# Optimization experiments

Hardware: AMD Instinct MI355X
Metric: run time of the kernel (lower is better)

The kernel has to match this reference:

```python
import jax, jax.numpy as jnp
import numpy as np

WAVE_LEN = 1000.0
DIM_G = 64


def box_relational_embedding(boxes):
    # boxes: (B, N, 4) -> (B, N, N, 64) trigonometric geometry embedding
    B, N, _ = boxes.shape
    x_min, y_min, x_max, y_max = jnp.split(boxes, 4, axis=-1)  # each (B,N,1)
    cx = (x_min + x_max) * 0.5
    cy = (y_min + y_max) * 0.5
    w = (x_max - x_min) + 1.0
    h = (y_max - y_min) + 1.0
    cxT = jnp.swapaxes(cx, 1, 2)  # (B,1,N)
    cyT = jnp.swapaxes(cy, 1, 2)
    dx = jnp.log(jnp.clip(jnp.abs((cx - cxT) / w), 1e-3))  # (B,N,N)
    dy = jnp.log(jnp.clip(jnp.abs((cy - cyT) / h), 1e-3))
    dw = jnp.log(w / jnp.swapaxes(w, 1, 2))
    dh = jnp.log(h / jnp.swapaxes(h, 1, 2))
    pos = jnp.stack([dx, dy, dw, dh], axis=-1)  # (B,N,N,4)
    n_freq = DIM_G // 8  # 8 frequency bands
    dim_mat = 1.0 / (WAVE_LEN ** (jnp.arange(n_freq, dtype=pos.dtype) / n_freq))
    mul = (100.0 * pos)[..., None] * dim_mat  # (B,N,N,4,8)
    mul = mul.reshape(B, N, N, 4 * n_freq)  # (B,N,N,32)
    return jnp.concatenate([jnp.sin(mul), jnp.cos(mul)], axis=-1)  # (B,N,N,64)


def setup_inputs() -> dict:
    key = jax.random.key(0)
    ks = jax.random.split(key, 12)
    B, N, D, H = 32, 196, 1024, 8
    scale = 0.02
    inp = {
        "input_query": jax.random.normal(ks[0], (B, N, D), jnp.float32),
        "input_key": jax.random.normal(ks[1], (B, N, D), jnp.float32),
        "input_value": jax.random.normal(ks[2], (B, N, D), jnp.float32),
        "input_box": jax.random.uniform(ks[3], (B, N, 4), jnp.float32),
        "Wq": jax.random.normal(ks[4], (D, D), jnp.float32) * scale,
        "bq": jnp.zeros((D,), jnp.float32),
        "Wk": jax.random.normal(ks[5], (D, D), jnp.float32) * scale,
        "bk": jnp.zeros((D,), jnp.float32),
        "Wv": jax.random.normal(ks[6], (D, D), jnp.float32) * scale,
        "bv": jnp.zeros((D,), jnp.float32),
        "Wo": jax.random.normal(ks[7], (D, D), jnp.float32) * scale,
        "bo": jnp.zeros((D,), jnp.float32),
        "WG_w": jax.random.normal(ks[8], (H, DIM_G), jnp.float32) * scale,  # 8 stacked (64->1) linears
        "WG_b": jnp.zeros((H,), jnp.float32),
    }
    return inp


def reference(input_query, input_key, input_value, input_box,
              Wq, bq, Wk, bk, Wv, bv, Wo, bo, WG_w, WG_b):
    B, N, D = input_query.shape
    H = WG_w.shape[0]
    dk = D // H
    # relation geometry weights per head: (B,H,N,N)
    geo = box_relational_embedding(input_box)  # (B,N,N,64)
    wg = jax.nn.relu(jnp.einsum('bnmg,hg->bhnm', geo, WG_w) + WG_b[None, :, None, None])
    # projections (torch Linear: x @ W.T + b), reshape to (B,H,N,dk)
    def proj(x, W, b):
        return (x @ W.T + b).reshape(B, N, H, dk).transpose(0, 2, 1, 3)
    q = proj(input_query, Wq, bq)
    k = proj(input_key, Wk, bk)
    v = proj(input_value, Wv, bv)
    scores = jnp.einsum('bhnd,bhmd->bhnm', q, k) / np.sqrt(dk).astype(q.dtype)
    logits = jnp.log(jnp.clip(wg, 1e-6)) + scores
    attn = jax.nn.softmax(logits, axis=-1)  # (B,H,N,N)
    out = jnp.einsum('bhnm,bhmd->bhnd', attn, v)  # (B,H,N,dk)
    out = out.transpose(0, 2, 1, 3).reshape(B, N, D)
    return out @ Wo.T + bo
```

## Files before the change

kernel.cpp:

```cpp
#include <hip/hip_runtime.h>
#include <hip/hip_bf16.h>

typedef __bf16 bf16;
typedef _Float16 half_t;
typedef bf16 bf16x8 __attribute__((ext_vector_type(8)));
typedef bf16 bf16x4 __attribute__((ext_vector_type(4)));
typedef float floatx4 __attribute__((ext_vector_type(4)));

#define B_ 32
#define N_ 196
#define H_ 8
#define D_ 1024
#define DK_ 128
#define BN_ (B_ * N_)
#define BH_ (B_ * H_)
#define NPAD_ 224
#define PSTRIDE_ 232

#define KT_ 16

typedef __attribute__((address_space(3))) unsigned int lds_uint;
typedef const __attribute__((address_space(1))) unsigned int glb_uint;

__device__ __forceinline__ void async_copy16(const bf16* g, bf16* l) {
  __builtin_amdgcn_global_load_lds((glb_uint*)g, (lds_uint*)l, 16, 0, 0);
}

__device__ __forceinline__ bf16x8 bzero8() {
  bf16x8 z;
#pragma unroll
  for (int i = 0; i < 8; i++) z[i] = (bf16)0.0f;
  return z;
}

#define BARRIER() asm volatile("s_barrier" ::: "memory")
#define WAITV0() asm volatile("s_waitcnt vmcnt(0)" ::: "memory")

__global__ __launch_bounds__(256) void cvt3_kernel(const float* __restrict__ s0,
                                                   const float* __restrict__ s1,
                                                   const float* __restrict__ s2,
                                                   bf16* __restrict__ d0,
                                                   bf16* __restrict__ d1,
                                                   bf16* __restrict__ d2, int n4) {
  const int which = blockIdx.y;
  const float* s = (which == 0) ? s0 : (which == 1) ? s1 : s2;
  bf16* d = (which == 0) ? d0 : (which == 1) ? d1 : d2;
  int i = blockIdx.x * 256 + threadIdx.x;
  if (i >= n4) return;
  float4 v = ((const float4*)s)[i];
  bf16x4 o;
  o[0] = (bf16)v.x;
  o[1] = (bf16)v.y;
  o[2] = (bf16)v.z;
  o[3] = (bf16)v.w;
  *(bf16x4*)(d + (size_t)i * 4) = o;
}

__global__ __launch_bounds__(256) void cvt4_kernel(const float* __restrict__ s0,
                                                   const float* __restrict__ s1,
                                                   const float* __restrict__ s2,
                                                   const float* __restrict__ s3,
                                                   bf16* __restrict__ d0,
                                                   bf16* __restrict__ d1,
                                                   bf16* __restrict__ d2,
                                                   bf16* __restrict__ d3, int n4) {
  const int which = blockIdx.y;
  const float* s = (which == 0) ? s0 : (which == 1) ? s1 : (which == 2) ? s2 : s3;
  bf16* d = (which == 0) ? d0 : (which == 1) ? d1 : (which == 2) ? d2 : d3;
  int i = blockIdx.x * 256 + threadIdx.x;
  if (i >= n4) return;
  float4 v = ((const float4*)s)[i];
  bf16x4 o;
  o[0] = (bf16)v.x;
  o[1] = (bf16)v.y;
  o[2] = (bf16)v.z;
  o[3] = (bf16)v.w;
  *(bf16x4*)(d + (size_t)i * 4) = o;
}

__global__ __launch_bounds__(256) void geo_kernel(const float* __restrict__ box,
                                                  const float* __restrict__ WGw,
                                                  const float* __restrict__ WGb,
                                                  half_t* __restrict__ S) {
  __shared__ float4 wsh[128];
  if (threadIdx.x < 128) wsh[threadIdx.x] = ((const float4*)WGw)[threadIdx.x];
  __syncthreads();

  int tid = blockIdx.x * 256 + threadIdx.x;
  int b = tid / (N_ * N_);
  int rem = tid - b * (N_ * N_);
  int n = rem / N_;
  int m = rem - n * N_;

  float4 bn = ((const float4*)box)[b * N_ + n];
  float4 bm = ((const float4*)box)[b * N_ + m];
  float cxn = (bn.x + bn.z) * 0.5f, cyn = (bn.y + bn.w) * 0.5f;
  float wn = bn.z - bn.x + 1.0f, hn = bn.w - bn.y + 1.0f;
  float cxm = (bm.x + bm.z) * 0.5f, cym = (bm.y + bm.w) * 0.5f;
  float wm = bm.z - bm.x + 1.0f, hm = bm.w - bm.y + 1.0f;

  float pos[4];
  pos[0] = __logf(fmaxf(fabsf((cxn - cxm) / wn), 1e-3f));
  pos[1] = __logf(fmaxf(fabsf((cyn - cym) / hn), 1e-3f));
  pos[2] = __logf(wn / wm);
  pos[3] = __logf(hn / hm);

  const float dims[8] = {1.0f,          0.4216965034f, 0.1778279410f, 0.0749894209f,
                         0.0316227766f, 0.0133352143f, 0.0056234133f, 0.0023713737f};
  float feat[64];
#pragma unroll
  for (int p = 0; p < 4; p++) {
#pragma unroll
    for (int f = 0; f < 8; f++) {
      float a = 100.0f * pos[p] * dims[f];
      feat[p * 8 + f] = __sinf(a);
      feat[32 + p * 8 + f] = __cosf(a);
    }
  }
#pragma unroll
  for (int hh = 0; hh < 8; hh++) {
    float accv = WGb[hh];
#pragma unroll
    for (int g4 = 0; g4 < 16; g4++) {
      float4 wv = wsh[hh * 16 + g4];
      accv += feat[g4 * 4 + 0] * wv.x + feat[g4 * 4 + 1] * wv.y +
              feat[g4 * 4 + 2] * wv.z + feat[g4 * 4 + 3] * wv.w;
    }
    S[((size_t)((b * H_ + hh) * N_ + n)) * NPAD_ + m] = (half_t)fmaxf(accv, 1e-6f);
  }
}

template <int VARIANT>
__global__ __launch_bounds__(256, 2) void gemm2p(
    const bf16* __restrict__ A0, const bf16* __restrict__ A1, const bf16* __restrict__ A2,
    const bf16* __restrict__ W0, const bf16* __restrict__ W1, const bf16* __restrict__ W2,
    const float* __restrict__ b0, const float* __restrict__ b1, const float* __restrict__ b2,
    void* __restrict__ O0, void* __restrict__ O1, void* __restrict__ O2) {
  __shared__ bf16 As[2][128 * 64];
  __shared__ bf16 Bs[2][128 * 64];

  const int z = (VARIANT == 0) ? blockIdx.z : 0;
  const bf16* A = (z == 0) ? A0 : (z == 1) ? A1 : A2;
  const bf16* W = (z == 0) ? W0 : (z == 1) ? W1 : W2;
  const float* bias = (z == 0) ? b0 : (z == 1) ? b1 : b2;

  const int tid = threadIdx.x;
  const int lane = tid & 63;
  const int wid = tid >> 6;
  const int l16 = lane & 15;
  const int quad = lane >> 4;
  const int wm = wid >> 1;
  const int wn = wid & 1;

  const bf16* gA = A + (size_t)blockIdx.y * 128 * D_;
  const bf16* gB = W + (size_t)blockIdx.x * 128 * D_;

  const int srow = tid >> 3;
  const int lslot = (tid & 7) ^ (srow & 7);
  size_t sOff[4];
#pragma unroll
  for (int u = 0; u < 4; u++) sOff[u] = (size_t)(u * 32 + srow) * D_ + lslot * 8;

  int arow[4], brow[4], kslot[2];
#pragma unroll
  for (int i = 0; i < 4; i++) arow[i] = (wm * 64 + i * 16 + l16) * 64;
#pragma unroll
  for (int j = 0; j < 4; j++) brow[j] = (wn * 64 + j * 16 + l16) * 64;
#pragma unroll
  for (int kk = 0; kk < 2; kk++) kslot[kk] = ((kk * 4 + quad) ^ (l16 & 7)) * 8;

  floatx4 acc[4][4];
#pragma unroll
  for (int i = 0; i < 4; i++)
#pragma unroll
    for (int j = 0; j < 4; j++)
#pragma unroll
      for (int r = 0; r < 4; r++) acc[i][j][r] = 0.0f;

#pragma unroll
  for (int u = 0; u < 4; u++) {
    async_copy16(gA + sOff[u], &As[0][u * 2048 + tid * 8]);
    async_copy16(gB + sOff[u], &Bs[0][u * 2048 + tid * 8]);
  }
  WAITV0();
  BARRIER();

  for (int kt = 0; kt < KT_; ++kt) {
    const int cur = kt & 1;
    const bf16* Ab = As[cur];
    const bf16* Bb = Bs[cur];
    const bool pf = (kt + 1 < KT_);
    const bf16* pa = gA + (kt + 1) * 64;
    const bf16* pb = gB + (kt + 1) * 64;
    bf16* dA = As[cur ^ 1];
    bf16* dB = Bs[cur ^ 1];
    bf16x8 af[4], bfv[4];

#pragma unroll
    for (int i = 0; i < 4; i++) af[i] = *(const bf16x8*)(Ab + arow[i] + kslot[0]);
#pragma unroll
    for (int j = 0; j < 4; j++) bfv[j] = *(const bf16x8*)(Bb + brow[j] + kslot[0]);
    if (pf) {
#pragma unroll
      for (int u = 0; u < 4; u++) async_copy16(pa + sOff[u], dA + u * 2048 + tid * 8);
    }
    __builtin_amdgcn_s_setprio(1);
#pragma unroll
    for (int i = 0; i < 4; i++)
#pragma unroll
      for (int j = 0; j < 4; j++)
        acc[i][j] = __builtin_amdgcn_mfma_f32_16x16x32_bf16(af[i], bfv[j], acc[i][j], 0, 0, 0);
    __builtin_amdgcn_s_setprio(0);

#pragma unroll
    for (int i = 0; i < 4; i++) af[i] = *(const bf16x8*)(Ab + arow[i] + kslot[1]);
#pragma unroll
    for (int j = 0; j < 4; j++) bfv[j] = *(const bf16x8*)(Bb + brow[j] + kslot[1]);
    if (pf) {
#pragma unroll
      for (int u = 0; u < 4; u++) async_copy16(pb + sOff[u], dB + u * 2048 + tid * 8);
    }
    __builtin_amdgcn_s_setprio(1);
#pragma unroll
    for (int i = 0; i < 4; i++)
#pragma unroll
      for (int j = 0; j < 4; j++)
        acc[i][j] = __builtin_amdgcn_mfma_f32_16x16x32_bf16(af[i], bfv[j], acc[i][j], 0, 0, 0);
    __builtin_amdgcn_s_setprio(0);

    if (pf) {
      WAITV0();
      BARRIER();
    }
  }

  const int m0 = blockIdx.y * 128 + wm * 64;
  const int n0 = blockIdx.x * 128 + wn * 64;
#pragma unroll
  for (int j = 0; j < 4; j++) {
    const int col = n0 + j * 16 + l16;
    const float bv = bias[col];
#pragma unroll
    for (int i = 0; i < 4; i++) {
#pragma unroll
      for (int r = 0; r < 4; r++) {
        const int row = m0 + i * 16 + quad * 4 + r;
        float v = acc[i][j][r] + bv;
        if (VARIANT == 1) {
          ((float*)O0)[(size_t)row * D_ + col] = v;
        } else if (z < 2) {
          bf16* Cout = z ? (bf16*)O1 : (bf16*)O0;
          Cout[(size_t)row * D_ + col] = (bf16)v;
        } else {
          int b = row / N_;
          int n = row - b * N_;
          int h = col >> 7;
          int d = col & (DK_ - 1);
          ((bf16*)O2)[((size_t)((b * H_ + h) * DK_ + d)) * NPAD_ + n] = (bf16)v;
        }
      }
    }
  }
}

__global__ __launch_bounds__(256) void attn_kernel(const bf16* __restrict__ Q,
                                                   const bf16* __restrict__ Kmat,
                                                   const bf16* __restrict__ Vt,
                                                   const half_t* __restrict__ Sb,
                                                   bf16* __restrict__ AO) {
  __shared__ bf16 Pl[4 * 16 * PSTRIDE_];

  const int f = blockIdx.x;
  const int tile = (f >> 3) & 3;
  const int bh = (f & 7) | ((f >> 5) << 3);
  const int b = bh >> 3;
  const int h = bh & 7;
  const int wave = threadIdx.x >> 6;
  const int lane = threadIdx.x & 63;
  const int l16 = lane & 15;
  const int quad = lane >> 4;
  const int nrb = tile * 64 + wave * 16;

  floatx4 S[14];
#pragma unroll
  for (int j = 0; j < 14; j++)
#pragma unroll
    for (int r = 0; r < 4; r++) S[j][r] = 0.0f;

  const int na = nrb + l16;
  const bool nav = na < N_;
  const bf16* aptr = Q + ((size_t)(b * N_ + (nav ? na : 0))) * D_ + h * DK_ + quad * 8;
  bf16x8 afr[4];
#pragma unroll
  for (int kk = 0; kk < 4; kk++) afr[kk] = nav ? *(const bf16x8*)(aptr + kk * 32) : bzero8();

#pragma unroll
  for (int j = 0; j < 14; j++) {
    const int m = j * 16 + l16;
    const bool mv = m < N_;
    const bf16* kp = Kmat + ((size_t)(b * N_ + (mv ? m : 0))) * D_ + h * DK_ + quad * 8;
#pragma unroll
    for (int kk = 0; kk < 4; kk++) {
      bf16x8 bb = mv ? *(const bf16x8*)(kp + kk * 32) : bzero8();
      __builtin_amdgcn_s_setprio(1);
      S[j] = __builtin_amdgcn_mfma_f32_16x16x32_bf16(afr[kk], bb, S[j], 0, 0, 0);
      __builtin_amdgcn_s_setprio(0);
    }
  }

  const float scale = 0.08838834764831845f;
  const half_t* bbase = Sb + ((size_t)bh * N_) * NPAD_;
  bf16* pw = Pl + wave * 16 * PSTRIDE_;
  float inv[4];
#pragma unroll
  for (int r = 0; r < 4; r++) {
    const int n = nrb + quad * 4 + r;
    const size_t brow = (size_t)(n < N_ ? n : 0) * NPAD_;
    float mx = S[0][r] * scale;
#pragma unroll
    for (int j = 0; j < 14; j++) {
      S[j][r] *= scale;
      mx = fmaxf(mx, S[j][r]);
    }
#pragma unroll
    for (int off = 1; off < 16; off <<= 1) mx = fmaxf(mx, __shfl_xor(mx, off, 64));
    float sum = 0.0f;
#pragma unroll
    for (int j = 0; j < 14; j++) {
      const int m = j * 16 + l16;
      float w = (m < N_) ? (float)bbase[brow + m] : 0.0f;
      float e = w * __expf(S[j][r] - mx);
      sum += e;
      pw[(quad * 4 + r) * PSTRIDE_ + m] = (bf16)e;
    }
#pragma unroll
    for (int off = 1; off < 16; off <<= 1) sum += __shfl_xor(sum, off, 64);
    inv[r] = 1.0f / sum;
  }
  __syncthreads();

  floatx4 O[8];
#pragma unroll
  for (int j2 = 0; j2 < 8; j2++)
#pragma unroll
    for (int r = 0; r < 4; r++) O[j2][r] = 0.0f;

  const bf16* vbase = Vt + (size_t)bh * DK_ * NPAD_ + quad * 8;
  const bf16* pr = pw + l16 * PSTRIDE_ + quad * 8;
#pragma unroll
  for (int k0 = 0; k0 < NPAD_; k0 += 32) {
    bf16x8 a = *(const bf16x8*)(pr + k0);
#pragma unroll
    for (int j2 = 0; j2 < 8; j2++) {
      bf16x8 bb = *(const bf16x8*)(vbase + (size_t)(j2 * 16 + l16) * NPAD_ + k0);
      __builtin_amdgcn_s_setprio(1);
      O[j2] = __builtin_amdgcn_mfma_f32_16x16x32_bf16(a, bb, O[j2], 0, 0, 0);
      __builtin_amdgcn_s_setprio(0);
    }
  }

#pragma unroll
  for (int r = 0; r < 4; r++) {
    const int n = nrb + quad * 4 + r;
    if (n < N_) {
#pragma unroll
      for (int j2 = 0; j2 < 8; j2++) {
        AO[((size_t)(b * N_ + n)) * D_ + h * DK_ + j2 * 16 + l16] = (bf16)(O[j2][r] * inv[r]);
      }
    }
  }
}

extern "C" void kernel_launch(void* const* d_in, const int* in_sizes, int n_in,
                              void* d_out, int out_size, void* d_ws, size_t ws_size,
                              hipStream_t stream) {
  const float* xq = (const float*)d_in[0];
  const float* xk = (const float*)d_in[1];
  const float* xv = (const float*)d_in[2];
  const float* box = (const float*)d_in[3];
  const float* Wq = (const float*)d_in[4];
  const float* bq = (const float*)d_in[5];
  const float* Wk = (const float*)d_in[6];
  const float* bk = (const float*)d_in[7];
  const float* Wv = (const float*)d_in[8];
  const float* bv = (const float*)d_in[9];
  const float* Wo = (const float*)d_in[10];
  const float* bo = (const float*)d_in[11];
  const float* WGw = (const float*)d_in[12];
  const float* WGb = (const float*)d_in[13];

  size_t off = 0;
  char* wsc = (char*)d_ws;
  auto alloc = [&](size_t bytes) -> void* {
    void* p = wsc + off;
    off += (bytes + 255) & ~(size_t)255;
    return p;
  };
  bf16* xq_b = (bf16*)alloc((size_t)BN_ * D_ * 2);
  bf16* xk_b = (bf16*)alloc((size_t)BN_ * D_ * 2);
  bf16* xv_b = (bf16*)alloc((size_t)BN_ * D_ * 2);
  bf16* wq_b = (bf16*)alloc((size_t)D_ * D_ * 2);
  bf16* wk_b = (bf16*)alloc((size_t)D_ * D_ * 2);
  bf16* wv_b = (bf16*)alloc((size_t)D_ * D_ * 2);
  bf16* wo_b = (bf16*)alloc((size_t)D_ * D_ * 2);
  bf16* q_b = (bf16*)alloc((size_t)BN_ * D_ * 2);
  bf16* k_b = (bf16*)alloc((size_t)BN_ * D_ * 2);
  bf16* vt_b = (bf16*)alloc((size_t)BH_ * DK_ * NPAD_ * 2);
  bf16* ao_b = (bf16*)alloc((size_t)BN_ * D_ * 2);
  half_t* S = (half_t*)alloc((size_t)BH_ * N_ * NPAD_ * 2);

  const int n4x = BN_ * D_ / 4;
  const int n4w = D_ * D_ / 4;
  dim3 g3(n4x / 256, 3, 1);
  cvt3_kernel<<<g3, 256, 0, stream>>>(xq, xk, xv, xq_b, xk_b, xv_b, n4x);
  dim3 g4(n4w / 256, 4, 1);
  cvt4_kernel<<<g4, 256, 0, stream>>>(Wq, Wk, Wv, Wo, wq_b, wk_b, wv_b, wo_b, n4w);

  geo_kernel<<<(B_ * N_ * N_) / 256, 256, 0, stream>>>(box, WGw, WGb, S);

  hipMemsetAsync(vt_b, 0, (size_t)BH_ * DK_ * NPAD_ * 2, stream);

  dim3 gqkv(D_ / 128, BN_ / 128, 3);
  gemm2p<0><<<gqkv, 256, 0, stream>>>(xq_b, xk_b, xv_b, wq_b, wk_b, wv_b, bq, bk, bv,
                                      q_b, k_b, vt_b);

  attn_kernel<<<1024, 256, 0, stream>>>(q_b, k_b, vt_b, S, ao_b);

  dim3 gout(D_ / 128, BN_ / 128, 1);
  gemm2p<1><<<gout, 256, 0, stream>>>(ao_b, nullptr, nullptr, wo_b, nullptr, nullptr,
                                      bo, nullptr, nullptr, d_out, nullptr, nullptr);
}
```

Measured before the change: 355.7 us.

## Triple-buffer GEMM with smaller K tiles and stage K/V through LDS in attention

```diff
diff --git a/kernel.cpp b/kernel.cpp
--- a/kernel.cpp
+++ b/kernel.cpp
@@ -17,7 +17,7 @@
 #define NPAD_ 224
 #define PSTRIDE_ 232
 
-#define KT_ 16
+#define KT3_ 32
 
 typedef __attribute__((address_space(3))) unsigned int lds_uint;
 typedef const __attribute__((address_space(1))) unsigned int glb_uint;
@@ -26,15 +26,9 @@
   __builtin_amdgcn_global_load_lds((glb_uint*)g, (lds_uint*)l, 16, 0, 0);
 }
 
-__device__ __forceinline__ bf16x8 bzero8() {
-  bf16x8 z;
-#pragma unroll
-  for (int i = 0; i < 8; i++) z[i] = (bf16)0.0f;
-  return z;
-}
-
 #define BARRIER() asm volatile("s_barrier" ::: "memory")
 #define WAITV0() asm volatile("s_waitcnt vmcnt(0)" ::: "memory")
+#define WAITV4() asm volatile("s_waitcnt vmcnt(4)" ::: "memory")
 
 __global__ __launch_bounds__(256) void cvt3_kernel(const float* __restrict__ s0,
                                                    const float* __restrict__ s1,
@@ -131,13 +125,13 @@
 }
 
 template <int VARIANT>
-__global__ __launch_bounds__(256, 2) void gemm2p(
+__global__ __launch_bounds__(256, 3) void gemm3b(
     const bf16* __restrict__ A0, const bf16* __restrict__ A1, const bf16* __restrict__ A2,
     const bf16* __restrict__ W0, const bf16* __restrict__ W1, const bf16* __restrict__ W2,
     const float* __restrict__ b0, const float* __restrict__ b1, const float* __restrict__ b2,
     void* __restrict__ O0, void* __restrict__ O1, void* __restrict__ O2) {
-  __shared__ bf16 As[2][128 * 64];
-  __shared__ bf16 Bs[2][128 * 64];
+  __shared__ bf16 As[3][128 * 32];
+  __shared__ bf16 Bs[3][128 * 32];
 
   const int z = (VARIANT == 0) ? blockIdx.z : 0;
   const bf16* A = (z == 0) ? A0 : (z == 1) ? A1 : A2;
@@ -155,19 +149,23 @@
   const bf16* gA = A + (size_t)blockIdx.y * 128 * D_;
   const bf16* gB = W + (size_t)blockIdx.x * 128 * D_;
 
-  const int srow = tid >> 3;
-  const int lslot = (tid & 7) ^ (srow & 7);
-  size_t sOff[4];
-#pragma unroll
-  for (int u = 0; u < 4; u++) sOff[u] = (size_t)(u * 32 + srow) * D_ + lslot * 8;
-
-  int arow[4], brow[4], kslot[2];
-#pragma unroll
-  for (int i = 0; i < 4; i++) arow[i] = (wm * 64 + i * 16 + l16) * 64;
-#pragma unroll
-  for (int j = 0; j < 4; j++) brow[j] = (wn * 64 + j * 16 + l16) * 64;
-#pragma unroll
-  for (int kk = 0; kk < 2; kk++) kslot[kk] = ((kk * 4 + quad) ^ (l16 & 7)) * 8;
+  size_t sOff[2];
+  int sDst[2];
+#pragma unroll
+  for (int u = 0; u < 2; u++) {
+    const int slot = u * 256 + tid;
+    const int srow = slot >> 2;
+    const int scs = slot & 3;
+    sOff[u] = (size_t)srow * D_ + (size_t)((scs ^ (srow & 3)) * 8);
+    sDst[u] = slot * 8;
+  }
+
+  int arow[4], brow[4];
+#pragma unroll
+  for (int i = 0; i < 4; i++) arow[i] = (wm * 64 + i * 16 + l16) * 32;
+#pragma unroll
+  for (int j = 0; j < 4; j++) brow[j] = (wn * 64 + j * 16 + l16) * 32;
+  const int kslot = (quad ^ (l16 & 3)) * 8;
 
   floatx4 acc[4][4];
 #pragma unroll
@@ -178,32 +176,38 @@
       for (int r = 0; r < 4; r++) acc[i][j][r] = 0.0f;
 
 #pragma unroll
-  for (int u = 0; u < 4; u++) {
-    async_copy16(gA + sOff[u], &As[0][u * 2048 + tid * 8]);
-    async_copy16(gB + sOff[u], &Bs[0][u * 2048 + tid * 8]);
-  }
-  WAITV0();
+  for (int kt = 0; kt < 2; kt++) {
+    const bf16* sa = gA + kt * 32;
+    const bf16* sb = gB + kt * 32;
+#pragma unroll
+    for (int u = 0; u < 2; u++) {
+      async_copy16(sa + sOff[u], &As[kt][sDst[u]]);
+      async_copy16(sb + sOff[u], &Bs[kt][sDst[u]]);
+    }
+  }
+  WAITV4();
   BARRIER();
 
-  for (int kt = 0; kt < KT_; ++kt) {
-    const int cur = kt & 1;
-    const bf16* Ab = As[cur];
-    const bf16* Bb = Bs[cur];
-    const bool pf = (kt + 1 < KT_);
-    const bf16* pa = gA + (kt + 1) * 64;
-    const bf16* pb = gB + (kt + 1) * 64;
-    bf16* dA = As[cur ^ 1];
-    bf16* dB = Bs[cur ^ 1];
+  for (int kt = 0; kt < KT3_; ++kt) {
+    const int g = kt % 3;
+    const bool pf = (kt + 2 < KT3_);
+    if (pf) {
+      const int gn = (kt + 2) % 3;
+      const bf16* pa = gA + (kt + 2) * 32;
+      const bf16* pb = gB + (kt + 2) * 32;
+#pragma unroll
+      for (int u = 0; u < 2; u++) {
+        async_copy16(pa + sOff[u], &As[gn][sDst[u]]);
+        async_copy16(pb + sOff[u], &Bs[gn][sDst[u]]);
+      }
+    }
+    const bf16* Ab = As[g];
+    const bf16* Bb = Bs[g];
     bf16x8 af[4], bfv[4];
-
-#pragma unroll
-    for (int i = 0; i < 4; i++) af[i] = *(const bf16x8*)(Ab + arow[i] + kslot[0]);
-#pragma unroll
-    for (int j = 0; j < 4; j++) bfv[j] = *(const bf16x8*)(Bb + brow[j] + kslot[0]);
-    if (pf) {
-#pragma unroll
-      for (int u = 0; u < 4; u++) async_copy16(pa + sOff[u], dA + u * 2048 + tid * 8);
-    }
+#pragma unroll
+    for (int i = 0; i < 4; i++) af[i] = *(const bf16x8*)(Ab + arow[i] + kslot);
+#pragma unroll
+    for (int j = 0; j < 4; j++) bfv[j] = *(const bf16x8*)(Bb + brow[j] + kslot);
     __builtin_amdgcn_s_setprio(1);
 #pragma unroll
     for (int i = 0; i < 4; i++)
@@ -211,25 +215,9 @@
       for (int j = 0; j < 4; j++)
         acc[i][j] = __builtin_amdgcn_mfma_f32_16x16x32_bf16(af[i], bfv[j], acc[i][j], 0, 0, 0);
     __builtin_amdgcn_s_setprio(0);
-
-#pragma unroll
-    for (int i = 0; i < 4; i++) af[i] = *(const bf16x8*)(Ab + arow[i] + kslot[1]);
-#pragma unroll
-    for (int j = 0; j < 4; j++) bfv[j] = *(const bf16x8*)(Bb + brow[j] + kslot[1]);
-    if (pf) {
-#pragma unroll
-      for (int u = 0; u < 4; u++) async_copy16(pb + sOff[u], dB + u * 2048 + tid * 8);
-    }
-    __builtin_amdgcn_s_setprio(1);
-#pragma unroll
-    for (int i = 0; i < 4; i++)
-#pragma unroll
-      for (int j = 0; j < 4; j++)
-        acc[i][j] = __builtin_amdgcn_mfma_f32_16x16x32_bf16(af[i], bfv[j], acc[i][j], 0, 0, 0);
-    __builtin_amdgcn_s_setprio(0);
-
-    if (pf) {
-      WAITV0();
+    if (kt < KT3_ - 1) {
+      if (pf) WAITV4();
+      else    WAITV0();
       BARRIER();
     }
   }
@@ -268,45 +256,97 @@
                                                    const bf16* __restrict__ Vt,
                                                    const half_t* __restrict__ Sb,
                                                    bf16* __restrict__ AO) {
-  __shared__ bf16 Pl[4 * 16 * PSTRIDE_];
+  __shared__ alignas(16) char smem[46080];
+  bf16* KsB[2] = {(bf16*)smem, (bf16*)smem + 4096};
+  bf16* Pl = (bf16*)smem;
+  bf16* VsB[2] = {(bf16*)(smem + 29696), (bf16*)(smem + 29696) + 4096};
 
   const int f = blockIdx.x;
   const int tile = (f >> 3) & 3;
   const int bh = (f & 7) | ((f >> 5) << 3);
   const int b = bh >> 3;
   const int h = bh & 7;
-  const int wave = threadIdx.x >> 6;
-  const int lane = threadIdx.x & 63;
+  const int tid = threadIdx.x;
+  const int wave = tid >> 6;
+  const int lane = tid & 63;
   const int l16 = lane & 15;
   const int quad = lane >> 4;
   const int nrb = tile * 64 + wave * 16;
 
-  floatx4 S[14];
-#pragma unroll
-  for (int j = 0; j < 14; j++)
-#pragma unroll
-    for (int r = 0; r < 4; r++) S[j][r] = 0.0f;
+  size_t kSrc[2];
+  int kDst[2];
+#pragma unroll
+  for (int u = 0; u < 2; u++) {
+    const int slot = u * 256 + tid;
+    const int srow = slot >> 4;
+    const int scs = slot & 15;
+    kSrc[u] = (size_t)(b * N_ + srow) * D_ + h * DK_ + (scs ^ (srow & 7)) * 8;
+    kDst[u] = slot * 8;
+  }
+  size_t vSrc[2];
+#pragma unroll
+  for (int u = 0; u < 2; u++) {
+    const int slot = u * 256 + tid;
+    const int vrow = slot >> 2;
+    const int vcs = slot & 3;
+    vSrc[u] = (size_t)bh * DK_ * NPAD_ + (size_t)vrow * NPAD_ + (vcs ^ (vrow & 3)) * 8;
+  }
+
+#pragma unroll
+  for (int u = 0; u < 2; u++) async_copy16(Kmat + kSrc[u], KsB[0] + kDst[u]);
 
   const int na = nrb + l16;
   const bool nav = na < N_;
   const bf16* aptr = Q + ((size_t)(b * N_ + (nav ? na : 0))) * D_ + h * DK_ + quad * 8;
   bf16x8 afr[4];
 #pragma unroll
-  for (int kk = 0; kk < 4; kk++) afr[kk] = nav ? *(const bf16x8*)(aptr + kk * 32) : bzero8();
-
-#pragma unroll
-  for (int j = 0; j < 14; j++) {
-    const int m = j * 16 + l16;
-    const bool mv = m < N_;
-    const bf16* kp = Kmat + ((size_t)(b * N_ + (mv ? m : 0))) * D_ + h * DK_ + quad * 8;
-#pragma unroll
-    for (int kk = 0; kk < 4; kk++) {
-      bf16x8 bb = mv ? *(const bf16x8*)(kp + kk * 32) : bzero8();
-      __builtin_amdgcn_s_setprio(1);
-      S[j] = __builtin_amdgcn_mfma_f32_16x16x32_bf16(afr[kk], bb, S[j], 0, 0, 0);
-      __builtin_amdgcn_s_setprio(0);
-    }
-  }
+  for (int kk = 0; kk < 4; kk++) {
+    bf16x8 v = *(const bf16x8*)(aptr + kk * 32);
+    if (!nav) {
+#pragma unroll
+      for (int e = 0; e < 8; e++) v[e] = (bf16)0.0f;
+    }
+    afr[kk] = v;
+  }
+  WAITV0();
+  BARRIER();
+
+  floatx4 S[14];
+#pragma unroll
+  for (int j = 0; j < 14; j++)
+#pragma unroll
+    for (int r = 0; r < 4; r++) S[j][r] = 0.0f;
+
+  for (int jt = 0; jt < 7; ++jt) {
+    const int cur = jt & 1;
+    if (jt < 6) {
+      const size_t koff = (size_t)((jt + 1) * 32) * D_;
+#pragma unroll
+      for (int u = 0; u < 2; u++)
+        async_copy16(Kmat + kSrc[u] + koff, KsB[cur ^ 1] + kDst[u]);
+    }
+    const bf16* Kb = KsB[cur];
+    __builtin_amdgcn_s_setprio(1);
+#pragma unroll
+    for (int jj = 0; jj < 2; jj++) {
+      const int mloc = jj * 16 + l16;
+#pragma unroll
+      for (int kk = 0; kk < 4; kk++) {
+        bf16x8 bb = *(const bf16x8*)(Kb + mloc * 128 + ((kk * 4 + quad) ^ (l16 & 7)) * 8);
+        S[jt * 2 + jj] = __builtin_amdgcn_mfma_f32_16x16x32_bf16(afr[kk], bb, S[jt * 2 + jj], 0, 0, 0);
+      }
+    }
+    __builtin_amdgcn_s_setprio(0);
+    if (jt < 6) {
+      WAITV0();
+      BARRIER();
+    }
+  }
+
+#pragma unroll
+  for (int u = 0; u < 2; u++) async_copy16(Vt + vSrc[u], VsB[0] + kDst[u]);
+
+  BARRIER();
 
   const float scale = 0.08838834764831845f;
   const half_t* bbase = Sb + ((size_t)bh * N_) * NPAD_;
@@ -315,12 +355,15 @@
 #pragma unroll
   for (int r = 0; r < 4; r++) {
     const int n = nrb + quad * 4 + r;
-    const size_t brow = (size_t)(n < N_ ? n : 0) * NPAD_;
-    float mx = S[0][r] * scale;
+    const bool nv = n < N_;
+    const size_t brow = (size_t)(nv ? n : 0) * NPAD_;
+    float mx = -1e30f;
 #pragma unroll
     for (int j = 0; j < 14; j++) {
-      S[j][r] *= scale;
-      mx = fmaxf(mx, S[j][r]);
+      const int m = j * 16 + l16;
+      float s = (nv && m < N_) ? S[j][r] * scale : -1e30f;
+      S[j][r] = s;
+      mx = fmaxf(mx, s);
     }
 #pragma unroll
     for (int off = 1; off < 16; off <<= 1) mx = fmaxf(mx, __shfl_xor(mx, off, 64));
@@ -345,17 +388,27 @@
 #pragma unroll
     for (int r = 0; r < 4; r++) O[j2][r] = 0.0f;
 
-  const bf16* vbase = Vt + (size_t)bh * DK_ * NPAD_ + quad * 8;
   const bf16* pr = pw + l16 * PSTRIDE_ + quad * 8;
-#pragma unroll
-  for (int k0 = 0; k0 < NPAD_; k0 += 32) {
-    bf16x8 a = *(const bf16x8*)(pr + k0);
+  for (int t7 = 0; t7 < 7; ++t7) {
+    const int cur = t7 & 1;
+    if (t7 < 6) {
+      const size_t voff = (size_t)((t7 + 1) * 32);
+#pragma unroll
+      for (int u = 0; u < 2; u++)
+        async_copy16(Vt + vSrc[u] + voff, VsB[cur ^ 1] + kDst[u]);
+    }
+    const bf16* Vb = VsB[cur];
+    bf16x8 a = *(const bf16x8*)(pr + t7 * 32);
+    __builtin_amdgcn_s_setprio(1);
 #pragma unroll
     for (int j2 = 0; j2 < 8; j2++) {
-      bf16x8 bb = *(const bf16x8*)(vbase + (size_t)(j2 * 16 + l16) * NPAD_ + k0);
-      __builtin_amdgcn_s_setprio(1);
+      bf16x8 bb = *(const bf16x8*)(Vb + (j2 * 16 + l16) * 32 + (quad ^ (l16 & 3)) * 8);
       O[j2] = __builtin_amdgcn_mfma_f32_16x16x32_bf16(a, bb, O[j2], 0, 0, 0);
-      __builtin_amdgcn_s_setprio(0);
+    }
+    __builtin_amdgcn_s_setprio(0);
+    if (t7 < 6) {
+      WAITV0();
+      BARRIER();
     }
   }
 
@@ -421,12 +474,12 @@
   hipMemsetAsync(vt_b, 0, (size_t)BH_ * DK_ * NPAD_ * 2, stream);
 
   dim3 gqkv(D_ / 128, BN_ / 128, 3);
-  gemm2p<0><<<gqkv, 256, 0, stream>>>(xq_b, xk_b, xv_b, wq_b, wk_b, wv_b, bq, bk, bv,
+  gemm3b<0><<<gqkv, 256, 0, stream>>>(xq_b, xk_b, xv_b, wq_b, wk_b, wv_b, bq, bk, bv,
                                       q_b, k_b, vt_b);
 
   attn_kernel<<<1024, 256, 0, stream>>>(q_b, k_b, vt_b, S, ao_b);
 
   dim3 gout(D_ / 128, BN_ / 128, 1);
-  gemm2p<1><<<gout, 256, 0, stream>>>(ao_b, nullptr, nullptr, wo_b, nullptr, nullptr,
+  gemm3b<1><<<gout, 256, 0, stream>>>(ao_b, nullptr, nullptr, wo_b, nullptr, nullptr,
                                       bo, nullptr, nullptr, d_out, nullptr, nullptr);
 }
```

After: 320.0 us. 1.11x faster.
